# Kernel tuning notes

Hardware: AMD Instinct MI355X
Metric: run time of the kernel (lower is better)

The kernel has to match this reference:

```python
import jax, jax.numpy as jnp
import numpy as np

# ---- static config matching init_kwargs ----
B, H, S, D = 1, 16, 8192, 64
BS = 64                  # block_size (= block_m = block_n here)
NB = S // BS             # 128 query/key blocks
LOCAL = 8                # local window width in blocks

# Block-level sparse pattern: causal, global block 0 + local window of 8 blocks.
_pat = np.zeros((NB, NB), dtype=bool)
for _i in range(NB):
    _pat[_i, 0] = True
    _pat[_i, max(0, _i - LOCAL + 1):_i + 1] = True
MAX_NNZ = int(_pat.sum(1).max())  # 9
_cols = np.zeros((NB, MAX_NNZ), np.int32)
_cmask = np.zeros((NB, MAX_NNZ), bool)
for _i in range(NB):
    _nz = np.nonzero(_pat[_i])[0]
    _cols[_i, :len(_nz)] = _nz
    _cmask[_i, :len(_nz)] = True
COLS = jnp.asarray(_cols)        # [NB, MAX_NNZ] padded column block indices
COLMASK = jnp.asarray(_cmask)    # [NB, MAX_NNZ] validity of padded entries
NEG_INF = jnp.float32(-1e30)


def setup_inputs() -> dict:
    key = jax.random.key(0)
    kq, kk, kv = jax.random.split(key, 3)
    q = jax.random.normal(kq, (B, H, S, D), dtype=jnp.float32)
    k = jax.random.normal(kk, (B, H, S, D), dtype=jnp.float32)
    v = jax.random.normal(kv, (B, H, S, D), dtype=jnp.float32)
    return {"q": q, "k": k, "v": v}


def reference(q, k, v):
    sm_scale = 1.0 / float(np.sqrt(D))
    qb = q.reshape(B, H, NB, BS, D)
    kb = k.reshape(B, H, NB, BS, D)
    vb = v.reshape(B, H, NB, BS, D)
    # gather only the nonzero key/value blocks per query block (honor sparsity)
    kg = kb[:, :, COLS]  # [B,H,NB,MAX_NNZ,BS,D]
    vg = vb[:, :, COLS]  # [B,H,NB,MAX_NNZ,BS,D]
    scores = jnp.einsum('bhimd,bhinjd->bhimnj', qb, kg) * sm_scale  # [B,H,NB,BS,MAX_NNZ,BS]
    # causal + padded-block mask
    q_pos = jnp.arange(NB, dtype=jnp.int32)[:, None] * BS + jnp.arange(BS, dtype=jnp.int32)[None, :]   # [NB,BS]
    k_pos = COLS[:, :, None] * BS + jnp.arange(BS, dtype=jnp.int32)                                     # [NB,MAX_NNZ,BS]
    mask = (k_pos[:, None, :, :] <= q_pos[:, :, None, None]) & COLMASK[:, None, :, None]                # [NB,BS,MAX_NNZ,BS]
    scores = jnp.where(mask, scores, NEG_INF)
    p = jax.nn.softmax(scores.reshape(B, H, NB, BS, MAX_NNZ * BS), axis=-1)
    out = jnp.einsum('bhimn,bhind->bhimd', p, vg.reshape(B, H, NB, MAX_NNZ * BS, D))
    return out.reshape(B, H, S, D)
```

## Files before the change

kernel.cpp:

```cpp
#include <hip/hip_runtime.h>
#include <hip/hip_bf16.h>
#include <string.h>

typedef __attribute__((ext_vector_type(8))) short short8;
typedef __attribute__((ext_vector_type(4))) float floatx4;

#define HH 16
#define SS 8192
#define DD 64
#define NBQ 128
#define LOG2E 1.44269504088896f

__device__ __forceinline__ unsigned pkbf(float a, float b) {
    __hip_bfloat162 h2 = __float22bfloat162_rn(make_float2(a, b));
    unsigned r;
    memcpy(&r, &h2, 4);
    return r;
}

__global__ __launch_bounds__(256, 4) void sparse_attn_kernel(
        const float* __restrict__ qg, const float* __restrict__ kg,
        const float* __restrict__ vg, float* __restrict__ og) {
    __shared__ unsigned short lds_k[2][64 * 64];
    __shared__ unsigned short lds_vt[2][64 * 64];
    __shared__ unsigned short lds_p[4][16 * 64];

    const int bid = (int)blockIdx.x;
    const int work = (bid & 7) * 256 + (bid >> 3);
    const int h = work >> 7;
    const int i = work & (NBQ - 1);
    const int tid = (int)threadIdx.x;
    const int w = tid >> 6;
    const int lane = tid & 63;
    const int lp = lane & 15;
    const int g = lane >> 4;

    const float* kh = kg + (size_t)h * SS * DD;
    const float* vh = vg + (size_t)h * SS * DD;

    short8 qf[2];
    {
        const float sc = 0.125f * LOG2E;
        const float* qrow = qg + ((size_t)h * SS + i * 64 + w * 16 + lp) * DD;
        #pragma unroll
        for (int f = 0; f < 2; ++f) {
            const float* p0 = qrow + f * 32 + 8 * g;
            float4 x = *(const float4*)(p0);
            float4 y = *(const float4*)(p0 + 4);
            union { unsigned u[4]; short8 s; } t_;
            t_.u[0] = pkbf(x.x * sc, x.y * sc);
            t_.u[1] = pkbf(x.z * sc, x.w * sc);
            t_.u[2] = pkbf(y.x * sc, y.y * sc);
            t_.u[3] = pkbf(y.z * sc, y.w * sc);
            qf[f] = t_.s;
        }
    }

    floatx4 acc[4];
    #pragma unroll
    for (int tt = 0; tt < 4; ++tt) acc[tt] = (floatx4)(0.f);
    float m = -1e30f;
    float lsum = 0.f;

    const int nnz = (i < 8) ? (i + 1) : 9;

    float4 kreg[4];
    float vreg[16];
    const int krow_sub = tid >> 4;
    const int kc4 = (tid & 15) * 4;

    {
        const float* kb = kh;
        const float* vb = vh;
        #pragma unroll
        for (int p = 0; p < 4; ++p)
            kreg[p] = *(const float4*)(kb + (p * 16 + krow_sub) * DD + kc4);
        #pragma unroll
        for (int kk = 0; kk < 16; ++kk)
            vreg[kk] = vb[(w * 16 + kk) * DD + lane];
    }

    const int swl = (lp & 7) << 3;

    for (int t = 0; t < nnz; ++t) {
        const int j = (i < 8) ? t : ((t == 0) ? 0 : (i - 8 + t));
        const int buf = t & 1;

        #pragma unroll
        for (int p = 0; p < 4; ++p) {
            const int row = p * 16 + krow_sub;
            uint2 pk;
            pk.x = pkbf(kreg[p].x, kreg[p].y);
            pk.y = pkbf(kreg[p].z, kreg[p].w);
            *(uint2*)(&lds_k[buf][row * 64 + (kc4 ^ ((row & 7) << 3))]) = pk;
        }
        {
            const int d = lane;
            const int sw = (d & 7) << 3;
            uint4 A, Bv;
            A.x = pkbf(vreg[0], vreg[1]);   A.y = pkbf(vreg[2], vreg[3]);
            A.z = pkbf(vreg[4], vreg[5]);   A.w = pkbf(vreg[6], vreg[7]);
            Bv.x = pkbf(vreg[8], vreg[9]);  Bv.y = pkbf(vreg[10], vreg[11]);
            Bv.z = pkbf(vreg[12], vreg[13]); Bv.w = pkbf(vreg[14], vreg[15]);
            *(uint4*)(&lds_vt[buf][d * 64 + ((w * 16) ^ sw)]) = A;
            *(uint4*)(&lds_vt[buf][d * 64 + ((w * 16 + 8) ^ sw)]) = Bv;
        }

        if (t + 1 < nnz) {
            const int jn = (i < 8) ? (t + 1) : (i - 8 + (t + 1));
            const float* kb = kh + jn * (64 * DD);
            const float* vb = vh + jn * (64 * DD);
            #pragma unroll
            for (int p = 0; p < 4; ++p)
                kreg[p] = *(const float4*)(kb + (p * 16 + krow_sub) * DD + kc4);
            #pragma unroll
            for (int kk = 0; kk < 16; ++kk)
                vreg[kk] = vb[(w * 16 + kk) * DD + lane];
        }

        __syncthreads();

        floatx4 st[4];
        #pragma unroll
        for (int kc = 0; kc < 4; ++kc) st[kc] = (floatx4)(0.f);
        #pragma unroll
        for (int kc = 0; kc < 4; ++kc) {
            const int row = kc * 16 + lp;
            const short8 kf0 = *(const short8*)(&lds_k[buf][row * 64 + ((8 * g) ^ swl)]);
            const short8 kf1 = *(const short8*)(&lds_k[buf][row * 64 + ((32 + 8 * g) ^ swl)]);
            st[kc] = __builtin_amdgcn_mfma_f32_16x16x32_bf16(kf0, qf[0], st[kc], 0, 0, 0);
            st[kc] = __builtin_amdgcn_mfma_f32_16x16x32_bf16(kf1, qf[1], st[kc], 0, 0, 0);
        }

        if (j == i) {
            #pragma unroll
            for (int kc = 0; kc < 4; ++kc) {
                #pragma unroll
                for (int r = 0; r < 4; ++r) {
                    const int key = kc * 16 + 4 * g + r;
                    if (key > w * 16 + lp) st[kc][r] = -1e30f;
                }
            }
        }

        float vmax = -1e30f;
        #pragma unroll
        for (int kc = 0; kc < 4; ++kc) {
            #pragma unroll
            for (int r = 0; r < 4; ++r) vmax = fmaxf(vmax, st[kc][r]);
        }
        vmax = fmaxf(vmax, __shfl_xor(vmax, 16));
        vmax = fmaxf(vmax, __shfl_xor(vmax, 32));
        const float m_new = fmaxf(m, vmax);
        const float alpha = exp2f(m - m_new);
        float psum = 0.f;
        #pragma unroll
        for (int kc = 0; kc < 4; ++kc) {
            #pragma unroll
            for (int r = 0; r < 4; ++r) {
                const float p = exp2f(st[kc][r] - m_new);
                st[kc][r] = p;
                psum += p;
            }
        }
        psum += __shfl_xor(psum, 16);
        psum += __shfl_xor(psum, 32);
        lsum = lsum * alpha + psum;
        m = m_new;
        #pragma unroll
        for (int tt = 0; tt < 4; ++tt) acc[tt] *= alpha;

        unsigned short* pw = lds_p[w];
        #pragma unroll
        for (int kc = 0; kc < 4; ++kc) {
            uint2 pk;
            pk.x = pkbf(st[kc][0], st[kc][1]);
            pk.y = pkbf(st[kc][2], st[kc][3]);
            const int e = lp * 64 + ((kc * 16 + 4 * g) ^ swl);
            *(uint2*)(&pw[e]) = pk;
        }

        const short8 pf0 = *(const short8*)(&pw[lp * 64 + ((8 * g) ^ swl)]);
        const short8 pf1 = *(const short8*)(&pw[lp * 64 + ((32 + 8 * g) ^ swl)]);
        #pragma unroll
        for (int tt = 0; tt < 4; ++tt) {
            const int row = tt * 16 + lp;
            const short8 vf0 = *(const short8*)(&lds_vt[buf][row * 64 + ((8 * g) ^ swl)]);
            const short8 vf1 = *(const short8*)(&lds_vt[buf][row * 64 + ((32 + 8 * g) ^ swl)]);
            acc[tt] = __builtin_amdgcn_mfma_f32_16x16x32_bf16(vf0, pf0, acc[tt], 0, 0, 0);
            acc[tt] = __builtin_amdgcn_mfma_f32_16x16x32_bf16(vf1, pf1, acc[tt], 0, 0, 0);
        }
    }

    const float rn = 1.0f / lsum;
    float* ob = og + ((size_t)h * SS + i * 64 + w * 16 + lp) * DD;
    #pragma unroll
    for (int tt = 0; tt < 4; ++tt) {
        float4 o4;
        o4.x = acc[tt][0] * rn;
        o4.y = acc[tt][1] * rn;
        o4.z = acc[tt][2] * rn;
        o4.w = acc[tt][3] * rn;
        *(float4*)(ob + tt * 16 + 4 * g) = o4;
    }
}

extern "C" void kernel_launch(void* const* d_in, const int* in_sizes, int n_in,
                              void* d_out, int out_size, void* d_ws, size_t ws_size,
                              hipStream_t stream) {
    const float* q = (const float*)d_in[0];
    const float* k = (const float*)d_in[1];
    const float* v = (const float*)d_in[2];
    float* out = (float*)d_out;
    dim3 grid(HH * NBQ);
    dim3 block(256);
    sparse_attn_kernel<<<grid, block, 0, stream>>>(q, k, v, out);
}
```

Baseline: 67.08 us.

## Pre-convert K/V to swizzled bf16 tiles and stream them via direct-to-LDS loads

Adds a prep kernel that converts each K and V block once to bf16, writing K in the swizzled LDS layout and V transposed, into workspace. The attention kernel then copies these ready-made tiles straight into LDS with global_load_lds, double-buffered. This removes the repeated fp32 loads and conversion of each K/V block, which the old kernel redid for every one of the up to 9 query blocks that use it, and it frees the registers that held the prefetched data. The cost is a second kernel launch, an extra pass over K and V, and a dependence on the workspace, with the old kernel kept as a fallback when the workspace is too small.

```diff
diff --git a/kernel.cpp b/kernel.cpp
--- a/kernel.cpp
+++ b/kernel.cpp
@@ -9,7 +9,10 @@
 #define SS 8192
 #define DD 64
 #define NBQ 128
+#define NTILE (HH * NBQ)
+#define TILE_ELEMS 4096
 #define LOG2E 1.44269504088896f
+#define WS_NEEDED ((size_t)NTILE * TILE_ELEMS * 2 * 2)
 
 __device__ __forceinline__ unsigned pkbf(float a, float b) {
     __hip_bfloat162 h2 = __float22bfloat162_rn(make_float2(a, b));
@@ -18,11 +21,70 @@
     return r;
 }
 
+__device__ __forceinline__ void gload16(const void* g, void* l) {
+    __builtin_amdgcn_global_load_lds(
+        (const __attribute__((address_space(1))) unsigned int*)g,
+        (__attribute__((address_space(3))) unsigned int*)l, 16, 0, 0);
+}
+
+__global__ __launch_bounds__(256, 4) void prep_kernel(
+        const float* __restrict__ kg, const float* __restrict__ vg,
+        unsigned short* __restrict__ kimg, unsigned short* __restrict__ vtimg) {
+    __shared__ float lv[64 * 64];
+    const int tile = (int)blockIdx.x;
+    const int tid = (int)threadIdx.x;
+    const float* kb = kg + (size_t)tile * TILE_ELEMS;
+    const float* vb = vg + (size_t)tile * TILE_ELEMS;
+    unsigned short* ko = kimg + (size_t)tile * TILE_ELEMS;
+    unsigned short* vo = vtimg + (size_t)tile * TILE_ELEMS;
+
+    const int row = tid >> 2;
+    const int c16 = (tid & 3) * 16;
+
+    {
+        const float* src = kb + row * 64 + c16;
+        float4 a = ((const float4*)src)[0];
+        float4 b = ((const float4*)src)[1];
+        float4 c = ((const float4*)src)[2];
+        float4 d = ((const float4*)src)[3];
+        uint4 lo, hi;
+        lo.x = pkbf(a.x, a.y); lo.y = pkbf(a.z, a.w);
+        lo.z = pkbf(b.x, b.y); lo.w = pkbf(b.z, b.w);
+        hi.x = pkbf(c.x, c.y); hi.y = pkbf(c.z, c.w);
+        hi.z = pkbf(d.x, d.y); hi.w = pkbf(d.z, d.w);
+        const int sw = (row & 7) << 3;
+        *(uint4*)(ko + row * 64 + (c16 ^ sw)) = lo;
+        *(uint4*)(ko + row * 64 + ((c16 + 8) ^ sw)) = hi;
+    }
+
+    {
+        const float4* src = (const float4*)(vb + row * 64 + c16);
+        float4* dst = (float4*)(&lv[row * 64 + c16]);
+        dst[0] = src[0]; dst[1] = src[1]; dst[2] = src[2]; dst[3] = src[3];
+    }
+    __syncthreads();
+    {
+        const int d = row;
+        const int kc16 = c16;
+        float x[16];
+        #pragma unroll
+        for (int kk = 0; kk < 16; ++kk) x[kk] = lv[(kc16 + kk) * 64 + d];
+        uint4 lo, hi;
+        lo.x = pkbf(x[0], x[1]);  lo.y = pkbf(x[2], x[3]);
+        lo.z = pkbf(x[4], x[5]);  lo.w = pkbf(x[6], x[7]);
+        hi.x = pkbf(x[8], x[9]);  hi.y = pkbf(x[10], x[11]);
+        hi.z = pkbf(x[12], x[13]); hi.w = pkbf(x[14], x[15]);
+        const int sw = (d & 7) << 3;
+        *(uint4*)(vo + d * 64 + (kc16 ^ sw)) = lo;
+        *(uint4*)(vo + d * 64 + ((kc16 + 8) ^ sw)) = hi;
+    }
+}
+
 __global__ __launch_bounds__(256, 4) void sparse_attn_kernel(
-        const float* __restrict__ qg, const float* __restrict__ kg,
-        const float* __restrict__ vg, float* __restrict__ og) {
-    __shared__ unsigned short lds_k[2][64 * 64];
-    __shared__ unsigned short lds_vt[2][64 * 64];
+        const float* __restrict__ qg, const unsigned short* __restrict__ kimg,
+        const unsigned short* __restrict__ vtimg, float* __restrict__ og) {
+    __shared__ unsigned short lds_k[2][TILE_ELEMS];
+    __shared__ unsigned short lds_vt[2][TILE_ELEMS];
     __shared__ unsigned short lds_p[4][16 * 64];
 
     const int bid = (int)blockIdx.x;
@@ -35,8 +97,8 @@
     const int lp = lane & 15;
     const int g = lane >> 4;
 
-    const float* kh = kg + (size_t)h * SS * DD;
-    const float* vh = vg + (size_t)h * SS * DD;
+    const unsigned short* ktiles = kimg + (size_t)h * NBQ * TILE_ELEMS;
+    const unsigned short* vtiles = vtimg + (size_t)h * NBQ * TILE_ELEMS;
 
     short8 qf[2];
     {
@@ -63,6 +125,162 @@
     float lsum = 0.f;
 
     const int nnz = (i < 8) ? (i + 1) : 9;
+    const int lane8 = lane * 8;
+
+    auto stage = [&](int j, int b) {
+        const unsigned short* ks = ktiles + (size_t)j * TILE_ELEMS + w * 512 + lane8;
+        const unsigned short* vs = vtiles + (size_t)j * TILE_ELEMS + w * 512 + lane8;
+        gload16(ks,        &lds_k[b][w * 512]);
+        gload16(ks + 2048, &lds_k[b][2048 + w * 512]);
+        gload16(vs,        &lds_vt[b][w * 512]);
+        gload16(vs + 2048, &lds_vt[b][2048 + w * 512]);
+    };
+
+    stage(0, 0);
+    __syncthreads();
+
+    const int swl = (lp & 7) << 3;
+
+    for (int t = 0; t < nnz; ++t) {
+        const int j = (i < 8) ? t : ((t == 0) ? 0 : (i - 8 + t));
+        const int buf = t & 1;
+
+        if (t + 1 < nnz) {
+            const int jn = (i < 8) ? (t + 1) : (i - 8 + (t + 1));
+            stage(jn, buf ^ 1);
+        }
+
+        floatx4 st[4];
+        #pragma unroll
+        for (int kc = 0; kc < 4; ++kc) st[kc] = (floatx4)(0.f);
+        #pragma unroll
+        for (int kc = 0; kc < 4; ++kc) {
+            const int row = kc * 16 + lp;
+            const short8 kf0 = *(const short8*)(&lds_k[buf][row * 64 + ((8 * g) ^ swl)]);
+            const short8 kf1 = *(const short8*)(&lds_k[buf][row * 64 + ((32 + 8 * g) ^ swl)]);
+            st[kc] = __builtin_amdgcn_mfma_f32_16x16x32_bf16(kf0, qf[0], st[kc], 0, 0, 0);
+            st[kc] = __builtin_amdgcn_mfma_f32_16x16x32_bf16(kf1, qf[1], st[kc], 0, 0, 0);
+        }
+
+        if (j == i) {
+            #pragma unroll
+            for (int kc = 0; kc < 4; ++kc) {
+                #pragma unroll
+                for (int r = 0; r < 4; ++r) {
+                    const int key = kc * 16 + 4 * g + r;
+                    if (key > w * 16 + lp) st[kc][r] = -1e30f;
+                }
+            }
+        }
+
+        float vmax = -1e30f;
+        #pragma unroll
+        for (int kc = 0; kc < 4; ++kc) {
+            #pragma unroll
+            for (int r = 0; r < 4; ++r) vmax = fmaxf(vmax, st[kc][r]);
+        }
+        vmax = fmaxf(vmax, __shfl_xor(vmax, 16));
+        vmax = fmaxf(vmax, __shfl_xor(vmax, 32));
+        const float m_new = fmaxf(m, vmax);
+        const float alpha = exp2f(m - m_new);
+        float psum = 0.f;
+        #pragma unroll
+        for (int kc = 0; kc < 4; ++kc) {
+            #pragma unroll
+            for (int r = 0; r < 4; ++r) {
+                const float p = exp2f(st[kc][r] - m_new);
+                st[kc][r] = p;
+                psum += p;
+            }
+        }
+        psum += __shfl_xor(psum, 16);
+        psum += __shfl_xor(psum, 32);
+        lsum = lsum * alpha + psum;
+        m = m_new;
+        #pragma unroll
+        for (int tt = 0; tt < 4; ++tt) acc[tt] *= alpha;
+
+        unsigned short* pw = lds_p[w];
+        #pragma unroll
+        for (int kc = 0; kc < 4; ++kc) {
+            uint2 pk;
+            pk.x = pkbf(st[kc][0], st[kc][1]);
+            pk.y = pkbf(st[kc][2], st[kc][3]);
+            const int e = lp * 64 + ((kc * 16 + 4 * g) ^ swl);
+            *(uint2*)(&pw[e]) = pk;
+        }
+
+        const short8 pf0 = *(const short8*)(&pw[lp * 64 + ((8 * g) ^ swl)]);
+        const short8 pf1 = *(const short8*)(&pw[lp * 64 + ((32 + 8 * g) ^ swl)]);
+        #pragma unroll
+        for (int tt = 0; tt < 4; ++tt) {
+            const int row = tt * 16 + lp;
+            const short8 vf0 = *(const short8*)(&lds_vt[buf][row * 64 + ((8 * g) ^ swl)]);
+            const short8 vf1 = *(const short8*)(&lds_vt[buf][row * 64 + ((32 + 8 * g) ^ swl)]);
+            acc[tt] = __builtin_amdgcn_mfma_f32_16x16x32_bf16(vf0, pf0, acc[tt], 0, 0, 0);
+            acc[tt] = __builtin_amdgcn_mfma_f32_16x16x32_bf16(vf1, pf1, acc[tt], 0, 0, 0);
+        }
+
+        if (t + 1 < nnz) __syncthreads();
+    }
+
+    const float rn = 1.0f / lsum;
+    float* ob = og + ((size_t)h * SS + i * 64 + w * 16 + lp) * DD;
+    #pragma unroll
+    for (int tt = 0; tt < 4; ++tt) {
+        float4 o4;
+        o4.x = acc[tt][0] * rn;
+        o4.y = acc[tt][1] * rn;
+        o4.z = acc[tt][2] * rn;
+        o4.w = acc[tt][3] * rn;
+        *(float4*)(ob + tt * 16 + 4 * g) = o4;
+    }
+}
+
+__global__ __launch_bounds__(256, 4) void sparse_attn_fb(
+        const float* __restrict__ qg, const float* __restrict__ kg,
+        const float* __restrict__ vg, float* __restrict__ og) {
+    __shared__ unsigned short lds_k[2][64 * 64];
+    __shared__ unsigned short lds_vt[2][64 * 64];
+    __shared__ unsigned short lds_p[4][16 * 64];
+
+    const int bid = (int)blockIdx.x;
+    const int work = (bid & 7) * 256 + (bid >> 3);
+    const int h = work >> 7;
+    const int i = work & (NBQ - 1);
+    const int tid = (int)threadIdx.x;
+    const int w = tid >> 6;
+    const int lane = tid & 63;
+    const int lp = lane & 15;
+    const int g = lane >> 4;
+
+    const float* kh = kg + (size_t)h * SS * DD;
+    const float* vh = vg + (size_t)h * SS * DD;
+
+    short8 qf[2];
+    {
+        const float sc = 0.125f * LOG2E;
+        const float* qrow = qg + ((size_t)h * SS + i * 64 + w * 16 + lp) * DD;
+        #pragma unroll
+        for (int f = 0; f < 2; ++f) {
+            const float* p0 = qrow + f * 32 + 8 * g;
+            float4 x = *(const float4*)(p0);
+            float4 y = *(const float4*)(p0 + 4);
+            union { unsigned u[4]; short8 s; } t_;
+            t_.u[0] = pkbf(x.x * sc, x.y * sc);
+            t_.u[1] = pkbf(x.z * sc, x.w * sc);
+            t_.u[2] = pkbf(y.x * sc, y.y * sc);
+            t_.u[3] = pkbf(y.z * sc, y.w * sc);
+            qf[f] = t_.s;
+        }
+    }
+
+    floatx4 acc[4];
+    #pragma unroll
+    for (int tt = 0; tt < 4; ++tt) acc[tt] = (floatx4)(0.f);
+    float m = -1e30f;
+    float lsum = 0.f;
+    const int nnz = (i < 8) ? (i + 1) : 9;
 
     float4 kreg[4];
     float vreg[16];
@@ -70,14 +288,12 @@
     const int kc4 = (tid & 15) * 4;
 
     {
-        const float* kb = kh;
-        const float* vb = vh;
         #pragma unroll
         for (int p = 0; p < 4; ++p)
-            kreg[p] = *(const float4*)(kb + (p * 16 + krow_sub) * DD + kc4);
+            kreg[p] = *(const float4*)(kh + (p * 16 + krow_sub) * DD + kc4);
         #pragma unroll
         for (int kk = 0; kk < 16; ++kk)
-            vreg[kk] = vb[(w * 16 + kk) * DD + lane];
+            vreg[kk] = vh[(w * 16 + kk) * DD + lane];
     }
 
     const int swl = (lp & 7) << 3;
@@ -212,7 +428,13 @@
     const float* k = (const float*)d_in[1];
     const float* v = (const float*)d_in[2];
     float* out = (float*)d_out;
-    dim3 grid(HH * NBQ);
-    dim3 block(256);
-    sparse_attn_kernel<<<grid, block, 0, stream>>>(q, k, v, out);
-}
+
+    if (ws_size >= WS_NEEDED) {
+        unsigned short* kimg = (unsigned short*)d_ws;
+        unsigned short* vtimg = kimg + (size_t)NTILE * TILE_ELEMS;
+        prep_kernel<<<dim3(NTILE), dim3(256), 0, stream>>>(k, v, kimg, vtimg);
+        sparse_attn_kernel<<<dim3(HH * NBQ), dim3(256), 0, stream>>>(q, kimg, vtimg, out);
+    } else {
+        sparse_attn_fb<<<dim3(HH * NBQ), dim3(256), 0, stream>>>(q, k, v, out);
+    }
+}
```

Result: slower. 69.70 us (+3.9%).
